# Kernel tuning notes

Measured on AMD Instinct MI355X. Metric: run time of the kernel, lower is better.

## Reference

```python
import jax, jax.numpy as jnp
import numpy as np

N = 32768          # nodes per graph (mol and protein must match for cat along dim 1)
E_MOL = 131072
E_PRO = 196608
F_MOL, F_PRO = 78, 54
HID, OUT_D, LAYERS = 512, 128, 3
ALPHA = 0.2


def _gcn_norm(edge_index, n, dtype):
    # add self loops, symmetric normalization D^-1/2 A D^-1/2 (PyG gcn_norm)
    sl = jnp.arange(n)
    row = jnp.concatenate([edge_index[0], sl])
    col = jnp.concatenate([edge_index[1], sl])
    deg = jax.ops.segment_sum(jnp.ones(row.shape[0], dtype), col, num_segments=n)
    dis = jnp.where(deg > 0, jax.lax.rsqrt(deg), 0.0).astype(dtype)
    return row, col, dis[row] * dis[col]


def _branch(x, edge_index, w_in, b_in, ws, w_out, b_out):
    # GCNII-dense stack: h = relu(Lin(x)); then per layer:
    #   agg = A_hat @ h ; support = (1-alpha)*agg + alpha*h0
    #   h = relu(support + support @ W_l) + h_prev   (identity-mapping + residual)
    n = x.shape[0]
    row, col, norm = _gcn_norm(edge_index, n, x.dtype)
    h = jax.nn.relu(x @ w_in + b_in)
    h0 = h
    prev = h
    for l in range(LAYERS):
        agg = jax.ops.segment_sum(norm[:, None] * prev[row], col, num_segments=n)  # [N,HID]
        support = (1.0 - ALPHA) * agg + ALPHA * h0
        prev = jax.nn.relu(support + support @ ws[l]) + prev
    return prev @ w_out + b_out  # [N, OUT_D]


def setup_inputs() -> dict:
    key = jax.random.key(0)
    ks = jax.random.split(key, 20)

    def glorot(k, shape):
        lim = float(np.sqrt(6.0 / (shape[-2] + shape[-1])))
        return jax.random.uniform(k, shape, jnp.float32, -lim, lim)

    inp = {
        "mol_x": jax.random.normal(ks[0], (N, F_MOL), jnp.float32),
        "mol_edge_index": jax.random.randint(ks[1], (2, E_MOL), 0, N, jnp.int64 if jax.config.jax_enable_x64 else jnp.int32),
        "pro_x": jax.random.normal(ks[2], (N, F_PRO), jnp.float32),
        "pro_edge_index": jax.random.randint(ks[3], (2, E_PRO), 0, N, jnp.int64 if jax.config.jax_enable_x64 else jnp.int32),
        "mol_w_in": glorot(ks[4], (F_MOL, HID)), "mol_b_in": jnp.zeros((HID,), jnp.float32),
        "mol_ws": glorot(ks[5], (LAYERS, HID, HID)),
        "mol_w_out": glorot(ks[6], (HID, OUT_D)), "mol_b_out": jnp.zeros((OUT_D,), jnp.float32),
        "pro_w_in": glorot(ks[7], (F_PRO, HID)), "pro_b_in": jnp.zeros((HID,), jnp.float32),
        "pro_ws": glorot(ks[8], (LAYERS, HID, HID)),
        "pro_w_out": glorot(ks[9], (HID, OUT_D)), "pro_b_out": jnp.zeros((OUT_D,), jnp.float32),
        "w_fc1": glorot(ks[10], (2 * OUT_D, 1024)), "b_fc1": jnp.zeros((1024,), jnp.float32),
        "w_fc2": glorot(ks[11], (1024, 512)), "b_fc2": jnp.zeros((512,), jnp.float32),
        "w_o": glorot(ks[12], (512, 1)), "b_o": jnp.zeros((1,), jnp.float32),
    }
    return inp


def reference(mol_x, mol_edge_index, pro_x, pro_edge_index,
              mol_w_in, mol_b_in, mol_ws, mol_w_out, mol_b_out,
              pro_w_in, pro_b_in, pro_ws, pro_w_out, pro_b_out,
              w_fc1, b_fc1, w_fc2, b_fc2, w_o, b_o):
    # eval mode: dropout = identity
    m = _branch(mol_x, mol_edge_index, mol_w_in, mol_b_in, mol_ws, mol_w_out, mol_b_out)
    p = _branch(pro_x, pro_edge_index, pro_w_in, pro_b_in, pro_ws, pro_w_out, pro_b_out)
    xc = jnp.concatenate([m, p], axis=1)            # [N, 2*OUT_D]
    xc = jax.nn.relu(xc @ w_fc1 + b_fc1)
    xc = jax.nn.relu(xc @ w_fc2 + b_fc2)
    return xc @ w_o + b_o                            # [N, 1]
```

## Files before the change

### kernel.cpp

```cpp
#include <hip/hip_runtime.h>
#include <stdint.h>

#define NN 32768
#define HID 512
#define EM 131072
#define EP 196608
#define AS1 __attribute__((address_space(1)))
#define AS3 __attribute__((address_space(3)))

typedef _Float16 h8 __attribute__((ext_vector_type(8)));
typedef float f4 __attribute__((ext_vector_type(4)));
typedef float f8 __attribute__((ext_vector_type(8)));

__device__ __forceinline__ void gload_lds16(const _Float16* g, _Float16* l) {
    __builtin_amdgcn_global_load_lds((AS1 void*)(g), (AS3 void*)(l), 16, 0, 0);
}
__device__ __forceinline__ f8 c8(h8 v) { return __builtin_convertvector(v, f8); }

struct ConvJobs {
    const float* src[12];
    _Float16* dst[12];
    int K[12], N[12], Kp[12];
    int blk0[13];
};

__global__ void conv_all(ConvJobs j) {
    __shared__ float tile[32][33];
    int blk = blockIdx.x, job = 0;
    while (blk >= j.blk0[job + 1]) ++job;
    int t = blk - j.blk0[job];
    int Kp = j.Kp[job], N = j.N[job], K = j.K[job];
    int ktiles = Kp >> 5;
    int n0 = (t / ktiles) << 5, k0 = (t % ktiles) << 5;
    int tn = threadIdx.x & 31, tr = threadIdx.x >> 5;
    const float* src = j.src[job];
    #pragma unroll
    for (int p = 0; p < 4; ++p) {
        int k = k0 + tr + p * 8;
        tile[tr + p * 8][tn] = (k < K) ? src[(size_t)k * N + n0 + tn] : 0.f;
    }
    __syncthreads();
    _Float16* dst = j.dst[job];
    #pragma unroll
    for (int p = 0; p < 4; ++p) {
        int nl = tr + p * 8;
        dst[((size_t)(k0 >> 5) * N + n0 + nl) * 32 + tn] = (_Float16)tile[tn][nl];
    }
}

__global__ void pad_x2(const float* s0, const float* s1, int F0, int F1, _Float16* dstb) {
    int z = blockIdx.z;
    const float* src = z ? s1 : s0;
    int F = z ? F1 : F0;
    _Float16* dst = dstb + (size_t)z * NN * 128;
    int idx = blockIdx.x * 256 + threadIdx.x;
    int i = idx >> 7, jj = idx & 127;
    dst[idx] = (jj < F) ? (_Float16)src[(size_t)i * F + jj] : (_Float16)0.f;
}

__global__ void init_deg(int* deg) {
    deg[(size_t)blockIdx.z * NN + blockIdx.x * 256 + threadIdx.x] = 1;
}

__global__ void count_edges2(const int* c0, int E0, const int* c1, int E1, int* deg) {
    int i = blockIdx.x * 256 + threadIdx.x;
    if (i < E0) atomicAdd(&deg[c0[i]], 1);
    else { i -= E0; if (i < E1) atomicAdd(&deg[NN + c1[i]], 1); }
}

__global__ void scan_offsets(const int* degb, int* offsb, int* curb, float* disb) {
    const int* deg = degb + blockIdx.z * NN;
    int* offs = offsb + blockIdx.z * (NN + 1);
    int* cur = curb + blockIdx.z * NN;
    float* dis = disb + blockIdx.z * NN;
    __shared__ int part[1024];
    int t = threadIdx.x, base = t * 32;
    int loc[32], sum = 0;
    for (int jj = 0; jj < 32; ++jj) {
        int d = deg[base + jj];
        dis[base + jj] = rsqrtf((float)d);
        loc[jj] = sum; sum += d - 1;
    }
    part[t] = sum;
    __syncthreads();
    for (int o = 1; o < 1024; o <<= 1) {
        int v = (t >= o) ? part[t - o] : 0;
        __syncthreads();
        part[t] += v;
        __syncthreads();
    }
    int pre = (t == 0) ? 0 : part[t - 1];
    for (int jj = 0; jj < 32; ++jj) { int x = pre + loc[jj]; offs[base + jj] = x; cur[base + jj] = x; }
    if (t == 1023) offs[NN] = part[1023];
}

__global__ void scatter2(const int* r0, const int* c0, int E0,
                         const int* r1, const int* c1, int E1,
                         int* cur, const float* dis, int2* s0, int2* s1) {
    int i = blockIdx.x * 256 + threadIdx.x;
    if (i < E0) {
        int r = r0[i];
        int p = atomicAdd(&cur[c0[i]], 1);
        int2 v; v.x = r; v.y = __float_as_int(dis[r]);
        s0[p] = v;
    } else {
        i -= E0;
        if (i < E1) {
            int r = r1[i];
            int p = atomicAdd(&cur[NN + c1[i]], 1);
            int2 v; v.x = r; v.y = __float_as_int(dis[NN + r]);
            s1[p] = v;
        }
    }
}

#define ROWP 536

struct LArgs {
    const _Float16* pin;
    const _Float16* h0;
    _Float16* pout;
    const float* dis;
    const int* offs;
    const int2* se0;
    const int2* se1;
    const _Float16* wT;
    const _Float16* woutT;
    const float* bo[2];
    _Float16* xc;
    size_t bstr;
    int mzadd;
};

__global__ __launch_bounds__(1024, 4) void layer_fused(LArgs a) {
    extern __shared__ _Float16 sup[];
    const int z = blockIdx.z, mz = z + a.mzadd;
    const _Float16* __restrict__ pin = a.pin + (size_t)z * a.bstr;
    const _Float16* __restrict__ h0 = a.h0 + (size_t)z * a.bstr;
    const _Float16* __restrict__ BT = a.wT + (size_t)z * (3 * 512 * 512);
    const float* __restrict__ dis = a.dis + mz * NN;
    const int* __restrict__ offs = a.offs + mz * (NN + 1);
    const int2* __restrict__ se = mz ? a.se1 : a.se0;
    const int tid = threadIdx.x, wave = tid >> 6, lane = tid & 63;
    const int row0 = blockIdx.x * 128;

    for (int i = 0; i < 8; ++i) {
        const int rl = wave * 8 + i, row = row0 + rl;
        const int e0 = offs[row], e1 = offs[row + 1];
        f8 acg = {};
        for (int e = e0; e < e1; e += 4) {
            const int j1 = (e + 1 < e1) ? e + 1 : e;
            const int j2 = (e + 2 < e1) ? e + 2 : e;
            const int j3 = (e + 3 < e1) ? e + 3 : e;
            const float m1 = (e + 1 < e1) ? 1.f : 0.f;
            const float m2 = (e + 2 < e1) ? 1.f : 0.f;
            const float m3 = (e + 3 < e1) ? 1.f : 0.f;
            const int2 p0 = se[e], p1 = se[j1], p2 = se[j2], p3 = se[j3];
            const float s0 = __int_as_float(p0.y);
            const float s1 = __int_as_float(p1.y) * m1;
            const float s2 = __int_as_float(p2.y) * m2;
            const float s3 = __int_as_float(p3.y) * m3;
            h8 v0 = *(const h8*)&pin[(size_t)p0.x * 512 + lane * 8];
            h8 v1 = *(const h8*)&pin[(size_t)p1.x * 512 + lane * 8];
            h8 v2 = *(const h8*)&pin[(size_t)p2.x * 512 + lane * 8];
            h8 v3 = *(const h8*)&pin[(size_t)p3.x * 512 + lane * 8];
            acg += s0 * c8(v0) + s1 * c8(v1) + s2 * c8(v2) + s3 * c8(v3);
        }
        const float si = dis[row];
        h8 pv = *(const h8*)&pin[(size_t)row * 512 + lane * 8];
        h8 hv = *(const h8*)&h0[(size_t)row * 512 + lane * 8];
        f8 r = 0.8f * si * (acg + si * c8(pv)) + 0.2f * c8(hv);
        *(h8*)&sup[rl * ROWP + lane * 8] = __builtin_convertvector(r, h8);
    }
    __syncthreads();

    const int wm = wave & 1, wn = wave >> 1;
    const int l15 = lane & 15, lq = lane >> 4;
    f4 acc[4][4] = {};
    #pragma unroll
    for (int kt = 0; kt < 8; ++kt) {
        #pragma unroll
        for (int s = 0; s < 2; ++s) {
            const int koff = kt * 64 + s * 32 + lq * 8;
            h8 af[4], bf[4];
            #pragma unroll
            for (int rt = 0; rt < 4; ++rt)
                af[rt] = *(const h8*)&sup[(wm * 64 + rt * 16 + l15) * ROWP + koff];
            #pragma unroll
            for (int ct = 0; ct < 4; ++ct)
                bf[ct] = *(const h8*)(BT + ((size_t)(kt * 2 + s) * 512
                                            + wn * 64 + ct * 16 + l15) * 32 + lq * 8);
            #pragma unroll
            for (int rt = 0; rt < 4; ++rt)
                #pragma unroll
                for (int ct = 0; ct < 4; ++ct)
                    acc[rt][ct] = __builtin_amdgcn_mfma_f32_16x16x32_f16(af[rt], bf[ct], acc[rt][ct], 0, 0, 0);
        }
    }
    __syncthreads();

    #pragma unroll
    for (int rt = 0; rt < 4; ++rt) {
        #pragma unroll
        for (int ct = 0; ct < 4; ++ct) {
            const int col = wn * 64 + ct * 16 + l15;
            #pragma unroll
            for (int r = 0; r < 4; ++r) {
                const int rl = wm * 64 + rt * 16 + lq * 4 + r;
                float nv = fmaxf((float)sup[rl * ROWP + col] + acc[rt][ct][r], 0.f);
                sup[rl * ROWP + col] = (_Float16)nv;
            }
        }
    }
    __syncthreads();

    const bool fuse_out = (a.woutT != nullptr);
    if (!fuse_out) {
        _Float16* __restrict__ pout = a.pout + (size_t)z * a.bstr;
        #pragma unroll
        for (int i = 0; i < 8; ++i) {
            const int rl = wave * 8 + i, row = row0 + rl;
            h8 s = *(const h8*)&sup[rl * ROWP + lane * 8];
            h8 pr = *(const h8*)&pin[(size_t)row * 512 + lane * 8];
            f8 v = c8(s) + c8(pr);
            *(h8*)&pout[(size_t)row * 512 + lane * 8] = __builtin_convertvector(v, h8);
        }
        return;
    }

    #pragma unroll
    for (int i = 0; i < 8; ++i) {
        const int rl = wave * 8 + i, row = row0 + rl;
        h8 s = *(const h8*)&sup[rl * ROWP + lane * 8];
        h8 pr = *(const h8*)&pin[(size_t)row * 512 + lane * 8];
        f8 v = c8(s) + c8(pr);
        *(h8*)&sup[rl * ROWP + lane * 8] = __builtin_convertvector(v, h8);
    }
    __syncthreads();

    const _Float16* __restrict__ WO = a.woutT + (size_t)z * (128 * 512);
    const float* __restrict__ bo = a.bo[mz];
    f4 acc2[4] = {};
    #pragma unroll
    for (int kt = 0; kt < 8; ++kt) {
        #pragma unroll
        for (int s = 0; s < 2; ++s) {
            const int koff = kt * 64 + s * 32 + lq * 8;
            h8 af[4];
            #pragma unroll
            for (int rt = 0; rt < 4; ++rt)
                af[rt] = *(const h8*)&sup[(wm * 64 + rt * 16 + l15) * ROWP + koff];
            h8 bf = *(const h8*)(WO + ((size_t)(kt * 2 + s) * 128 + wn * 16 + l15) * 32 + lq * 8);
            #pragma unroll
            for (int rt = 0; rt < 4; ++rt)
                acc2[rt] = __builtin_amdgcn_mfma_f32_16x16x32_f16(af[rt], bf, acc2[rt], 0, 0, 0);
        }
    }
    __syncthreads();
    #pragma unroll
    for (int rt = 0; rt < 4; ++rt) {
        const int col = wn * 16 + l15;
        #pragma unroll
        for (int r = 0; r < 4; ++r) {
            const int rl = wm * 64 + rt * 16 + lq * 4 + r;
            sup[rl * 136 + col] = (_Float16)(acc2[rt][r] + bo[col]);
        }
    }
    __syncthreads();
    #pragma unroll
    for (int i = 0; i < 2; ++i) {
        const int rl = wave * 8 + i * 4 + (lane >> 4);
        const int co = lane & 15;
        *(h8*)&a.xc[(size_t)(row0 + rl) * 256 + mz * 128 + co * 8] =
            *(const h8*)&sup[rl * 136 + co * 8];
    }
}

struct GArgs {
    const _Float16* A[2];
    const _Float16* BT[2];
    const float* bias[2];
    _Float16* C[2];
    _Float16* C2[2];
};

template <int K>
__global__ __launch_bounds__(512, 4) void gemm_a1(GArgs g, int ldc) {
    constexpr int NK = K / 64;
    __shared__ _Float16 lA[NK * 8 * 128 * 8];
    const int z = blockIdx.z;
    const _Float16* __restrict__ A = g.A[z];
    const _Float16* __restrict__ BT = g.BT[z];
    const int tid = threadIdx.x, wave = tid >> 6, lane = tid & 63;
    const int row0 = blockIdx.x * 128, col0 = blockIdx.y * 256;
    const int wm = wave & 1, wn = wave >> 1;
    const int l15 = lane & 15, lq = lane >> 4;
    constexpr int CNT = NK * 16 / 8;
    #pragma unroll
    for (int q = 0; q < CNT; ++q) {
        const int c = wave * CNT + q;
        const int kc = c >> 4, rem = c & 15, k8 = rem & 7, rh = rem >> 3;
        gload_lds16(A + (size_t)(row0 + rh * 64 + lane) * K + kc * 64 + k8 * 8,
                    &lA[((kc * 8 + k8) * 128 + rh * 64) * 8]);
    }
    __syncthreads();
    f4 acc[4][4] = {};
    #pragma unroll
    for (int kt = 0; kt < NK; ++kt) {
        #pragma unroll
        for (int s = 0; s < 2; ++s) {
            const int kq = s * 4 + lq;
            h8 af[4], bf[4];
            #pragma unroll
            for (int rt = 0; rt < 4; ++rt)
                af[rt] = *(const h8*)&lA[((kt * 8 + kq) * 128 + wm * 64 + rt * 16 + l15) * 8];
            #pragma unroll
            for (int ct = 0; ct < 4; ++ct)
                bf[ct] = *(const h8*)(BT + ((size_t)(kt * 2 + s) * ldc
                                            + col0 + wn * 64 + ct * 16 + l15) * 32 + lq * 8);
            #pragma unroll
            for (int rt = 0; rt < 4; ++rt)
                #pragma unroll
                for (int ct = 0; ct < 4; ++ct)
                    acc[rt][ct] = __builtin_amdgcn_mfma_f32_16x16x32_f16(af[rt], bf[ct], acc[rt][ct], 0, 0, 0);
        }
    }
    #pragma unroll
    for (int rt = 0; rt < 4; ++rt) {
        #pragma unroll
        for (int ct = 0; ct < 4; ++ct) {
            const int col = col0 + wn * 64 + ct * 16 + l15;
            #pragma unroll
            for (int r = 0; r < 4; ++r) {
                const int row = row0 + wm * 64 + rt * 16 + lq * 4 + r;
                float v = fmaxf(acc[rt][ct][r] + g.bias[z][col], 0.f);
                g.C[z][(size_t)row * ldc + col] = (_Float16)v;
                if (g.C2[z]) g.C2[z][(size_t)row * ldc + col] = (_Float16)v;
            }
        }
    }
}

__global__ __launch_bounds__(1024, 4) void gemm_fc2f(
    const _Float16* __restrict__ A, const _Float16* __restrict__ BT,
    const float* __restrict__ b2, const float* __restrict__ wo,
    const float* __restrict__ bo, float* __restrict__ out) {
    extern __shared__ _Float16 lA[];
    float* part = (float*)(lA + 64 * 1024);
    const int tid = threadIdx.x, wave = tid >> 6, lane = tid & 63;
    const int row0 = blockIdx.x * 64;
    const int wm = wave & 1, wn = wave >> 1;
    const int l15 = lane & 15, lq = lane >> 4;
    #pragma unroll
    for (int q = 0; q < 8; ++q) {
        const int c = wave * 8 + q;
        gload_lds16(A + (size_t)(row0 + lane) * 1024 + c * 8, &lA[(c * 64) * 8]);
    }
    __syncthreads();
    f4 acc[2][4] = {};
    #pragma unroll
    for (int kt = 0; kt < 32; ++kt) {
        const int ko = kt * 4 + lq;
        h8 af[2], bf[4];
        #pragma unroll
        for (int rt = 0; rt < 2; ++rt)
            af[rt] = *(const h8*)&lA[(ko * 64 + wm * 32 + rt * 16 + l15) * 8];
        #pragma unroll
        for (int ct = 0; ct < 4; ++ct)
            bf[ct] = *(const h8*)(BT + ((size_t)kt * 512 + wn * 64 + ct * 16 + l15) * 32 + lq * 8);
        #pragma unroll
        for (int rt = 0; rt < 2; ++rt)
            #pragma unroll
            for (int ct = 0; ct < 4; ++ct)
                acc[rt][ct] = __builtin_amdgcn_mfma_f32_16x16x32_f16(af[rt], bf[ct], acc[rt][ct], 0, 0, 0);
    }
    #pragma unroll
    for (int rt = 0; rt < 2; ++rt) {
        #pragma unroll
        for (int r = 0; r < 4; ++r) {
            float p = 0.f;
            #pragma unroll
            for (int ct = 0; ct < 4; ++ct) {
                const int colg = wn * 64 + ct * 16 + l15;
                float v = fmaxf(acc[rt][ct][r] + b2[colg], 0.f);
                p += v * wo[colg];
            }
            p += __shfl_xor(p, 1); p += __shfl_xor(p, 2);
            p += __shfl_xor(p, 4); p += __shfl_xor(p, 8);
            if (l15 == 0) {
                const int rl = wm * 32 + rt * 16 + lq * 4 + r;
                part[rl * 8 + wn] = p;
            }
        }
    }
    __syncthreads();
    if (tid < 64) {
        float s = bo[0];
        #pragma unroll
        for (int q = 0; q < 8; ++q) s += part[tid * 8 + q];
        out[row0 + tid] = s;
    }
}

struct WS {
    int *deg, *offs, *cur;
    int2 *srow0, *srow1;
    float* dis;
    _Float16 *winT, *wsT, *woutT, *fc1T, *fc2T;
    _Float16 *xpad, *h0, *prev0, *prev1, *xc;
    size_t total;
};

static WS plan(char* base, bool comb) {
    size_t off = 0;
    auto al = [&](size_t n) { off = (off + 255) & ~(size_t)255; size_t o = off; off += n; return base + o; };
    WS w;
    w.deg   = (int*)al(2 * NN * 4);
    w.dis   = (float*)al(2 * NN * 4);
    w.offs  = (int*)al(2 * (NN + 1) * 4);
    w.cur   = (int*)al(2 * NN * 4);
    w.srow0 = (int2*)al((size_t)EM * 8);
    w.srow1 = (int2*)al((size_t)EP * 8);
    w.winT  = (_Float16*)al(2 * 512 * 128 * 2);
    w.wsT   = (_Float16*)al((size_t)2 * 3 * 512 * 512 * 2);
    w.woutT = (_Float16*)al(2 * 128 * 512 * 2);
    w.fc1T  = (_Float16*)al(1024 * 256 * 2);
    w.fc2T  = (_Float16*)al((size_t)512 * 1024 * 2);
    const size_t nb = comb ? 2 : 1;
    const size_t HB = (size_t)NN * HID * 2;
    w.xpad  = (_Float16*)al(nb * NN * 128 * 2);
    w.h0    = (_Float16*)al(nb * HB);
    w.prev0 = (_Float16*)al(nb * HB);
    w.prev1 = (_Float16*)al(nb * HB);
    w.xc    = (_Float16*)al((size_t)NN * 256 * 2);
    w.total = off;
    return w;
}

extern "C" void kernel_launch(void* const* d_in, const int* in_sizes, int n_in,
                              void* d_out, int out_size, void* d_ws, size_t ws_size,
                              hipStream_t stream) {
    const float* mol_x   = (const float*)d_in[0];
    const int*   mol_ei  = (const int*)d_in[1];
    const float* pro_x   = (const float*)d_in[2];
    const int*   pro_ei  = (const int*)d_in[3];
    const float* win[2]  = {(const float*)d_in[4], (const float*)d_in[9]};
    const float* bin[2]  = {(const float*)d_in[5], (const float*)d_in[10]};
    const float* ws3[2]  = {(const float*)d_in[6], (const float*)d_in[11]};
    const float* wo[2]   = {(const float*)d_in[7], (const float*)d_in[12]};
    const float* bo[2]   = {(const float*)d_in[8], (const float*)d_in[13]};
    const float* w_fc1   = (const float*)d_in[14];
    const float* b_fc1   = (const float*)d_in[15];
    const float* w_fc2   = (const float*)d_in[16];
    const float* b_fc2   = (const float*)d_in[17];
    const float* w_o     = (const float*)d_in[18];
    const float* b_o     = (const float*)d_in[19];
    const int F[2] = {78, 54};

    char* wsb = (char*)d_ws;
    WS w = plan(wsb, true);
    const bool comb = (w.total <= ws_size);
    if (!comb) w = plan(wsb, false);
    const size_t BSTR = comb ? (size_t)NN * HID : 0;
    const size_t XSTR = comb ? (size_t)NN * 128 : 0;
    const int LDSB = 128 * ROWP * 2;
    const int LDSF = 64 * 1024 * 2 + 64 * 8 * 4;

    hipFuncSetAttribute((const void*)layer_fused,
                        hipFuncAttributeMaxDynamicSharedMemorySize, LDSB);
    hipFuncSetAttribute((const void*)gemm_fc2f,
                        hipFuncAttributeMaxDynamicSharedMemorySize, LDSF);

    ConvJobs j;
    int nblk = 0, ji = 0;
    auto addjob = [&](const float* s, _Float16* d, int K, int N, int Kp) {
        j.src[ji] = s; j.dst[ji] = d; j.K[ji] = K; j.N[ji] = N; j.Kp[ji] = Kp;
        j.blk0[ji] = nblk; nblk += (N >> 5) * (Kp >> 5); ++ji;
    };
    for (int b = 0; b < 2; ++b) addjob(win[b], w.winT + b * 512 * 128, F[b], 512, 128);
    for (int b = 0; b < 2; ++b)
        for (int l = 0; l < 3; ++l)
            addjob(ws3[b] + (size_t)l * 512 * 512,
                   w.wsT + ((size_t)b * 3 + l) * 512 * 512, 512, 512, 512);
    for (int b = 0; b < 2; ++b) addjob(wo[b], w.woutT + b * 128 * 512, 512, 128, 512);
    addjob(w_fc1, w.fc1T, 256, 1024, 256);
    addjob(w_fc2, w.fc2T, 1024, 512, 1024);
    j.blk0[12] = nblk;
    conv_all<<<nblk, 256, 0, stream>>>(j);

    init_deg<<<dim3(NN / 256, 1, 2), 256, 0, stream>>>(w.deg);
    count_edges2<<<(EM + EP + 255) / 256, 256, 0, stream>>>(mol_ei + EM, EM, pro_ei + EP, EP, w.deg);
    scan_offsets<<<dim3(1, 1, 2), 1024, 0, stream>>>(w.deg, w.offs, w.cur, w.dis);
    scatter2<<<(EM + EP + 255) / 256, 256, 0, stream>>>(mol_ei, mol_ei + EM, EM,
                                                        pro_ei, pro_ei + EP, EP,
                                                        w.cur, w.dis, w.srow0, w.srow1);

    auto branch_chain = [&](int zcount, int b0) {
        GArgs g{};
        for (int z = 0; z < zcount; ++z) {
            int b = b0 + z;
            g.A[z] = w.xpad + z * XSTR;
            g.BT[z] = w.winT + b * 512 * 128;
            g.bias[z] = bin[b];
            g.C[z] = w.h0 + z * BSTR;
            g.C2[z] = nullptr;
        }
        gemm_a1<128><<<dim3(256, 2, zcount), 512, 0, stream>>>(g, HID);
        const _Float16* pins[3] = {w.h0, w.prev1, w.prev0};
        _Float16* pouts[3] = {w.prev1, w.prev0, nullptr};
        for (int l = 0; l < 3; ++l) {
            LArgs a{};
            a.pin = pins[l];
            a.h0 = w.h0;
            a.pout = pouts[l];
            a.dis = w.dis; a.offs = w.offs;
            a.se0 = w.srow0; a.se1 = w.srow1;
            a.wT = w.wsT + ((size_t)b0 * 3 + l) * 512 * 512;
            a.woutT = (l == 2) ? (w.woutT + (size_t)b0 * 128 * 512) : nullptr;
            a.bo[0] = bo[0]; a.bo[1] = bo[1];
            a.xc = w.xc;
            a.bstr = BSTR; a.mzadd = b0;
            layer_fused<<<dim3(256, 1, zcount), 1024, LDSB, stream>>>(a);
        }
    };

    if (comb) {
        pad_x2<<<dim3(NN * 128 / 256, 1, 2), 256, 0, stream>>>(mol_x, pro_x, F[0], F[1], w.xpad);
        branch_chain(2, 0);
    } else {
        for (int b = 0; b < 2; ++b) {
            pad_x2<<<dim3(NN * 128 / 256, 1, 1), 256, 0, stream>>>(
                b ? pro_x : mol_x, nullptr, F[b], 0, w.xpad);
            branch_chain(1, b);
        }
    }

    _Float16* x1 = w.h0;
    GArgs g1{};
    g1.A[0] = w.xc; g1.BT[0] = w.fc1T; g1.bias[0] = b_fc1; g1.C[0] = x1; g1.C2[0] = nullptr;
    gemm_a1<256><<<dim3(256, 4, 1), 512, 0, stream>>>(g1, 1024);
    gemm_fc2f<<<dim3(NN / 64, 1), 1024, LDSF, stream>>>(x1, w.fc2T, b_fc2, w_o, b_o, (float*)d_out);
    (void)in_sizes; (void)n_in; (void)out_size; (void)ws_size;
}
```

Before: 681.0 us.

## Split fused layer into two half-tiles to overlap gather with MFMA

The fused GCN layer kernel now processes its 128-row tile as two 64-row halves in separate LDS buffers. The second half's sparse neighbour gather is issued before the first half's MFMA GEMM, so memory-bound gather work and matrix math from different waves can interleave. Each wave now covers 32 output columns across all 64 rows instead of 64x64, which changes the register and B-operand load pattern. The risk is that the gather and GEMM phases within a wave still run in sequence, so any overlap relies on the scheduler interleaving waves.

```diff
diff --git a/kernel.cpp b/kernel.cpp
--- a/kernel.cpp
+++ b/kernel.cpp
@@ -115,6 +115,7 @@
 }
 
 #define ROWP 536
+#define HROWS 64
 
 struct LArgs {
     const _Float16* pin;
@@ -133,7 +134,9 @@
 };
 
 __global__ __launch_bounds__(1024, 4) void layer_fused(LArgs a) {
-    extern __shared__ _Float16 sup[];
+    extern __shared__ _Float16 lds[];
+    _Float16* bufA = lds;
+    _Float16* bufB = lds + HROWS * ROWP;
     const int z = blockIdx.z, mz = z + a.mzadd;
     const _Float16* __restrict__ pin = a.pin + (size_t)z * a.bstr;
     const _Float16* __restrict__ h0 = a.h0 + (size_t)z * a.bstr;
@@ -143,103 +146,128 @@
     const int2* __restrict__ se = mz ? a.se1 : a.se0;
     const int tid = threadIdx.x, wave = tid >> 6, lane = tid & 63;
     const int row0 = blockIdx.x * 128;
-
-    for (int i = 0; i < 8; ++i) {
-        const int rl = wave * 8 + i, row = row0 + rl;
-        const int e0 = offs[row], e1 = offs[row + 1];
-        f8 acg = {};
-        for (int e = e0; e < e1; e += 4) {
-            const int j1 = (e + 1 < e1) ? e + 1 : e;
-            const int j2 = (e + 2 < e1) ? e + 2 : e;
-            const int j3 = (e + 3 < e1) ? e + 3 : e;
-            const float m1 = (e + 1 < e1) ? 1.f : 0.f;
-            const float m2 = (e + 2 < e1) ? 1.f : 0.f;
-            const float m3 = (e + 3 < e1) ? 1.f : 0.f;
-            const int2 p0 = se[e], p1 = se[j1], p2 = se[j2], p3 = se[j3];
-            const float s0 = __int_as_float(p0.y);
-            const float s1 = __int_as_float(p1.y) * m1;
-            const float s2 = __int_as_float(p2.y) * m2;
-            const float s3 = __int_as_float(p3.y) * m3;
-            h8 v0 = *(const h8*)&pin[(size_t)p0.x * 512 + lane * 8];
-            h8 v1 = *(const h8*)&pin[(size_t)p1.x * 512 + lane * 8];
-            h8 v2 = *(const h8*)&pin[(size_t)p2.x * 512 + lane * 8];
-            h8 v3 = *(const h8*)&pin[(size_t)p3.x * 512 + lane * 8];
-            acg += s0 * c8(v0) + s1 * c8(v1) + s2 * c8(v2) + s3 * c8(v3);
-        }
-        const float si = dis[row];
-        h8 pv = *(const h8*)&pin[(size_t)row * 512 + lane * 8];
-        h8 hv = *(const h8*)&h0[(size_t)row * 512 + lane * 8];
-        f8 r = 0.8f * si * (acg + si * c8(pv)) + 0.2f * c8(hv);
-        *(h8*)&sup[rl * ROWP + lane * 8] = __builtin_convertvector(r, h8);
-    }
-    __syncthreads();
-
-    const int wm = wave & 1, wn = wave >> 1;
     const int l15 = lane & 15, lq = lane >> 4;
-    f4 acc[4][4] = {};
-    #pragma unroll
-    for (int kt = 0; kt < 8; ++kt) {
-        #pragma unroll
-        for (int s = 0; s < 2; ++s) {
-            const int koff = kt * 64 + s * 32 + lq * 8;
-            h8 af[4], bf[4];
-            #pragma unroll
-            for (int rt = 0; rt < 4; ++rt)
-                af[rt] = *(const h8*)&sup[(wm * 64 + rt * 16 + l15) * ROWP + koff];
-            #pragma unroll
-            for (int ct = 0; ct < 4; ++ct)
-                bf[ct] = *(const h8*)(BT + ((size_t)(kt * 2 + s) * 512
-                                            + wn * 64 + ct * 16 + l15) * 32 + lq * 8);
-            #pragma unroll
-            for (int rt = 0; rt < 4; ++rt)
+
+    auto gather4 = [&](_Float16* buf, int rbase) {
+        for (int i = 0; i < 4; ++i) {
+            const int rl = wave * 4 + i, row = row0 + rbase + rl;
+            const int e0 = offs[row], e1 = offs[row + 1];
+            f8 acg = {};
+            for (int e = e0; e < e1; e += 4) {
+                const int j1 = (e + 1 < e1) ? e + 1 : e;
+                const int j2 = (e + 2 < e1) ? e + 2 : e;
+                const int j3 = (e + 3 < e1) ? e + 3 : e;
+                const float m1 = (e + 1 < e1) ? 1.f : 0.f;
+                const float m2 = (e + 2 < e1) ? 1.f : 0.f;
+                const float m3 = (e + 3 < e1) ? 1.f : 0.f;
+                const int2 p0 = se[e], p1 = se[j1], p2 = se[j2], p3 = se[j3];
+                const float s0 = __int_as_float(p0.y);
+                const float s1 = __int_as_float(p1.y) * m1;
+                const float s2 = __int_as_float(p2.y) * m2;
+                const float s3 = __int_as_float(p3.y) * m3;
+                h8 v0 = *(const h8*)&pin[(size_t)p0.x * 512 + lane * 8];
+                h8 v1 = *(const h8*)&pin[(size_t)p1.x * 512 + lane * 8];
+                h8 v2 = *(const h8*)&pin[(size_t)p2.x * 512 + lane * 8];
+                h8 v3 = *(const h8*)&pin[(size_t)p3.x * 512 + lane * 8];
+                acg += s0 * c8(v0) + s1 * c8(v1) + s2 * c8(v2) + s3 * c8(v3);
+            }
+            const float si = dis[row];
+            h8 pv = *(const h8*)&pin[(size_t)row * 512 + lane * 8];
+            h8 hv = *(const h8*)&h0[(size_t)row * 512 + lane * 8];
+            f8 r = 0.8f * si * (acg + si * c8(pv)) + 0.2f * c8(hv);
+            *(h8*)&buf[rl * ROWP + lane * 8] = __builtin_convertvector(r, h8);
+        }
+    };
+
+    auto gemmh = [&](const _Float16* buf, f4 (&acc)[4][2]) {
+        #pragma unroll
+        for (int kt = 0; kt < 8; ++kt) {
+            #pragma unroll
+            for (int s = 0; s < 2; ++s) {
+                const int koff = kt * 64 + s * 32 + lq * 8;
+                h8 af[4], bf[2];
                 #pragma unroll
-                for (int ct = 0; ct < 4; ++ct)
-                    acc[rt][ct] = __builtin_amdgcn_mfma_f32_16x16x32_f16(af[rt], bf[ct], acc[rt][ct], 0, 0, 0);
-        }
-    }
-    __syncthreads();
-
-    #pragma unroll
-    for (int rt = 0; rt < 4; ++rt) {
-        #pragma unroll
-        for (int ct = 0; ct < 4; ++ct) {
-            const int col = wn * 64 + ct * 16 + l15;
-            #pragma unroll
-            for (int r = 0; r < 4; ++r) {
-                const int rl = wm * 64 + rt * 16 + lq * 4 + r;
-                float nv = fmaxf((float)sup[rl * ROWP + col] + acc[rt][ct][r], 0.f);
-                sup[rl * ROWP + col] = (_Float16)nv;
+                for (int rt = 0; rt < 4; ++rt)
+                    af[rt] = *(const h8*)&buf[(rt * 16 + l15) * ROWP + koff];
+                #pragma unroll
+                for (int ct = 0; ct < 2; ++ct)
+                    bf[ct] = *(const h8*)(BT + ((size_t)(kt * 2 + s) * 512
+                                                + wave * 32 + ct * 16 + l15) * 32 + lq * 8);
+                #pragma unroll
+                for (int rt = 0; rt < 4; ++rt)
+                    #pragma unroll
+                    for (int ct = 0; ct < 2; ++ct)
+                        acc[rt][ct] = __builtin_amdgcn_mfma_f32_16x16x32_f16(af[rt], bf[ct], acc[rt][ct], 0, 0, 0);
             }
         }
-    }
+    };
+
+    auto epih = [&](_Float16* buf, f4 (&acc)[4][2]) {
+        #pragma unroll
+        for (int rt = 0; rt < 4; ++rt) {
+            #pragma unroll
+            for (int ct = 0; ct < 2; ++ct) {
+                const int col = wave * 32 + ct * 16 + l15;
+                #pragma unroll
+                for (int r = 0; r < 4; ++r) {
+                    const int rl = rt * 16 + lq * 4 + r;
+                    float nv = fmaxf((float)buf[rl * ROWP + col] + acc[rt][ct][r], 0.f);
+                    buf[rl * ROWP + col] = (_Float16)nv;
+                }
+            }
+        }
+    };
+
+    auto copyh = [&](const _Float16* buf, int rbase, _Float16* pout) {
+        #pragma unroll
+        for (int i = 0; i < 4; ++i) {
+            const int rl = wave * 4 + i, row = row0 + rbase + rl;
+            h8 s = *(const h8*)&buf[rl * ROWP + lane * 8];
+            h8 pr = *(const h8*)&pin[(size_t)row * 512 + lane * 8];
+            f8 v = c8(s) + c8(pr);
+            *(h8*)&pout[(size_t)row * 512 + lane * 8] = __builtin_convertvector(v, h8);
+        }
+    };
+
+    f4 accA[4][2] = {}, accB[4][2] = {};
+
+    gather4(bufA, 0);
+    __syncthreads();
+    gather4(bufB, 64);
+    gemmh(bufA, accA);
+    __syncthreads();
+    gemmh(bufB, accB);
+    epih(bufA, accA);
     __syncthreads();
 
     const bool fuse_out = (a.woutT != nullptr);
     if (!fuse_out) {
         _Float16* __restrict__ pout = a.pout + (size_t)z * a.bstr;
-        #pragma unroll
-        for (int i = 0; i < 8; ++i) {
-            const int rl = wave * 8 + i, row = row0 + rl;
-            h8 s = *(const h8*)&sup[rl * ROWP + lane * 8];
-            h8 pr = *(const h8*)&pin[(size_t)row * 512 + lane * 8];
-            f8 v = c8(s) + c8(pr);
-            *(h8*)&pout[(size_t)row * 512 + lane * 8] = __builtin_convertvector(v, h8);
-        }
+        epih(bufB, accB);
+        copyh(bufA, 0, pout);
+        __syncthreads();
+        copyh(bufB, 64, pout);
         return;
     }
 
+    epih(bufB, accB);
+    __syncthreads();
     #pragma unroll
     for (int i = 0; i < 8; ++i) {
-        const int rl = wave * 8 + i, row = row0 + rl;
-        h8 s = *(const h8*)&sup[rl * ROWP + lane * 8];
+        const int rloc = wave * 8 + i;
+        _Float16* buf = (rloc < 64) ? bufA : bufB;
+        const int rl = rloc & 63, row = row0 + rloc;
+        h8 s = *(const h8*)&buf[rl * ROWP + lane * 8];
         h8 pr = *(const h8*)&pin[(size_t)row * 512 + lane * 8];
         f8 v = c8(s) + c8(pr);
-        *(h8*)&sup[rl * ROWP + lane * 8] = __builtin_convertvector(v, h8);
+        *(h8*)&buf[rl * ROWP + lane * 8] = __builtin_convertvector(v, h8);
     }
     __syncthreads();
 
     const _Float16* __restrict__ WO = a.woutT + (size_t)z * (128 * 512);
     const float* __restrict__ bo = a.bo[mz];
+    const int wm = wave & 1, wn = wave >> 1;
+    const _Float16* bsel = wm ? bufB : bufA;
     f4 acc2[4] = {};
     #pragma unroll
     for (int kt = 0; kt < 8; ++kt) {
@@ -249,7 +277,7 @@
             h8 af[4];
             #pragma unroll
             for (int rt = 0; rt < 4; ++rt)
-                af[rt] = *(const h8*)&sup[(wm * 64 + rt * 16 + l15) * ROWP + koff];
+                af[rt] = *(const h8*)&bsel[(rt * 16 + l15) * ROWP + koff];
             h8 bf = *(const h8*)(WO + ((size_t)(kt * 2 + s) * 128 + wn * 16 + l15) * 32 + lq * 8);
             #pragma unroll
             for (int rt = 0; rt < 4; ++rt)
@@ -263,7 +291,7 @@
         #pragma unroll
         for (int r = 0; r < 4; ++r) {
             const int rl = wm * 64 + rt * 16 + lq * 4 + r;
-            sup[rl * 136 + col] = (_Float16)(acc2[rt][r] + bo[col]);
+            lds[rl * 136 + col] = (_Float16)(acc2[rt][r] + bo[col]);
         }
     }
     __syncthreads();
@@ -272,7 +300,7 @@
         const int rl = wave * 8 + i * 4 + (lane >> 4);
         const int co = lane & 15;
         *(h8*)&a.xc[(size_t)(row0 + rl) * 256 + mz * 128 + co * 8] =
-            *(const h8*)&sup[rl * 136 + co * 8];
+            *(const h8*)&lds[rl * 136 + co * 8];
     }
 }
 
```

After: 707.8 us. +3.9%, slower.

## Fuse fc1 and fc2 head GEMMs into one kernel keeping fc1 activations in LDS

Applied to the files above, without the earlier changes.

Replaces the separate fc1 GEMM kernel and the fc2+output kernel with one fused head kernel. Each 64-row block computes fc1 in 128-column chunks, writes the ReLU result to LDS as fp16, and immediately accumulates it into the fc2 product. This removes the global write and re-read of the N×1024 fc1 activation and one kernel launch. In exchange it adds two block barriers per chunk and loads the fc1 weights separately in every block.

```diff
diff --git a/kernel.cpp b/kernel.cpp
--- a/kernel.cpp
+++ b/kernel.cpp
@@ -341,38 +341,77 @@
     }
 }
 
-__global__ __launch_bounds__(1024, 4) void gemm_fc2f(
-    const _Float16* __restrict__ A, const _Float16* __restrict__ BT,
+__global__ __launch_bounds__(1024, 4) void head_fused(
+    const _Float16* __restrict__ xc, const _Float16* __restrict__ W1T,
+    const float* __restrict__ b1, const _Float16* __restrict__ W2T,
     const float* __restrict__ b2, const float* __restrict__ wo,
     const float* __restrict__ bo, float* __restrict__ out) {
-    extern __shared__ _Float16 lA[];
-    float* part = (float*)(lA + 64 * 1024);
+    __shared__ _Float16 lxc[32 * 64 * 8];
+    __shared__ _Float16 lx1[16 * 64 * 8];
+    __shared__ float part[64 * 8];
     const int tid = threadIdx.x, wave = tid >> 6, lane = tid & 63;
     const int row0 = blockIdx.x * 64;
     const int wm = wave & 1, wn = wave >> 1;
     const int l15 = lane & 15, lq = lane >> 4;
     #pragma unroll
-    for (int q = 0; q < 8; ++q) {
-        const int c = wave * 8 + q;
-        gload_lds16(A + (size_t)(row0 + lane) * 1024 + c * 8, &lA[(c * 64) * 8]);
-    }
-    __syncthreads();
-    f4 acc[2][4] = {};
-    #pragma unroll
-    for (int kt = 0; kt < 32; ++kt) {
-        const int ko = kt * 4 + lq;
-        h8 af[2], bf[4];
-        #pragma unroll
-        for (int rt = 0; rt < 2; ++rt)
-            af[rt] = *(const h8*)&lA[(ko * 64 + wm * 32 + rt * 16 + l15) * 8];
-        #pragma unroll
-        for (int ct = 0; ct < 4; ++ct)
-            bf[ct] = *(const h8*)(BT + ((size_t)kt * 512 + wn * 64 + ct * 16 + l15) * 32 + lq * 8);
-        #pragma unroll
-        for (int rt = 0; rt < 2; ++rt)
-            #pragma unroll
-            for (int ct = 0; ct < 4; ++ct)
-                acc[rt][ct] = __builtin_amdgcn_mfma_f32_16x16x32_f16(af[rt], bf[ct], acc[rt][ct], 0, 0, 0);
+    for (int q = 0; q < 2; ++q) {
+        const int c = wave * 2 + q;
+        gload_lds16(xc + (size_t)(row0 + lane) * 256 + c * 8, &lxc[(c * 64) * 8]);
+    }
+    __syncthreads();
+    f4 acc2[2][4] = {};
+    for (int cc = 0; cc < 8; ++cc) {
+        f4 acc1[2] = {};
+        #pragma unroll
+        for (int kt = 0; kt < 4; ++kt) {
+            #pragma unroll
+            for (int s = 0; s < 2; ++s) {
+                const int kq = s * 4 + lq;
+                h8 af[2];
+                #pragma unroll
+                for (int rt = 0; rt < 2; ++rt)
+                    af[rt] = *(const h8*)&lxc[((kt * 8 + kq) * 64 + wm * 32 + rt * 16 + l15) * 8];
+                const int col = cc * 128 + wn * 16 + l15;
+                h8 bf = *(const h8*)(W1T + ((size_t)(kt * 2 + s) * 1024 + col) * 32 + lq * 8);
+                #pragma unroll
+                for (int rt = 0; rt < 2; ++rt)
+                    acc1[rt] = __builtin_amdgcn_mfma_f32_16x16x32_f16(af[rt], bf, acc1[rt], 0, 0, 0);
+            }
+        }
+        __syncthreads();
+        {
+            const int cl = wn * 16 + l15;
+            const float bb = b1[cc * 128 + cl];
+            #pragma unroll
+            for (int rt = 0; rt < 2; ++rt)
+                #pragma unroll
+                for (int r = 0; r < 4; ++r) {
+                    const int row = wm * 32 + rt * 16 + lq * 4 + r;
+                    lx1[((cl >> 3) * 64 + row) * 8 + (cl & 7)] =
+                        (_Float16)fmaxf(acc1[rt][r] + bb, 0.f);
+                }
+        }
+        __syncthreads();
+        #pragma unroll
+        for (int kt = 0; kt < 2; ++kt) {
+            #pragma unroll
+            for (int s = 0; s < 2; ++s) {
+                const int kq = s * 4 + lq;
+                h8 af[2], bf[4];
+                #pragma unroll
+                for (int rt = 0; rt < 2; ++rt)
+                    af[rt] = *(const h8*)&lx1[((kt * 8 + kq) * 64 + wm * 32 + rt * 16 + l15) * 8];
+                #pragma unroll
+                for (int ct = 0; ct < 4; ++ct)
+                    bf[ct] = *(const h8*)(W2T + ((size_t)(cc * 4 + kt * 2 + s) * 512
+                                                 + wn * 64 + ct * 16 + l15) * 32 + lq * 8);
+                #pragma unroll
+                for (int rt = 0; rt < 2; ++rt)
+                    #pragma unroll
+                    for (int ct = 0; ct < 4; ++ct)
+                        acc2[rt][ct] = __builtin_amdgcn_mfma_f32_16x16x32_f16(af[rt], bf[ct], acc2[rt][ct], 0, 0, 0);
+            }
+        }
     }
     #pragma unroll
     for (int rt = 0; rt < 2; ++rt) {
@@ -382,7 +421,7 @@
             #pragma unroll
             for (int ct = 0; ct < 4; ++ct) {
                 const int colg = wn * 64 + ct * 16 + l15;
-                float v = fmaxf(acc[rt][ct][r] + b2[colg], 0.f);
+                float v = fmaxf(acc2[rt][ct][r] + b2[colg], 0.f);
                 p += v * wo[colg];
             }
             p += __shfl_xor(p, 1); p += __shfl_xor(p, 2);
@@ -464,12 +503,9 @@
     const size_t BSTR = comb ? (size_t)NN * HID : 0;
     const size_t XSTR = comb ? (size_t)NN * 128 : 0;
     const int LDSB = 128 * ROWP * 2;
-    const int LDSF = 64 * 1024 * 2 + 64 * 8 * 4;
 
     hipFuncSetAttribute((const void*)layer_fused,
                         hipFuncAttributeMaxDynamicSharedMemorySize, LDSB);
-    hipFuncSetAttribute((const void*)gemm_fc2f,
-                        hipFuncAttributeMaxDynamicSharedMemorySize, LDSF);
 
     ConvJobs j;
     int nblk = 0, ji = 0;
@@ -535,10 +571,7 @@
         }
     }
 
-    _Float16* x1 = w.h0;
-    GArgs g1{};
-    g1.A[0] = w.xc; g1.BT[0] = w.fc1T; g1.bias[0] = b_fc1; g1.C[0] = x1; g1.C2[0] = nullptr;
-    gemm_a1<256><<<dim3(256, 4, 1), 512, 0, stream>>>(g1, 1024);
-    gemm_fc2f<<<dim3(NN / 64, 1), 1024, LDSF, stream>>>(x1, w.fc2T, b_fc2, w_o, b_o, (float*)d_out);
+    head_fused<<<dim3(NN / 64, 1), 1024, 0, stream>>>(
+        w.xc, w.fc1T, b_fc1, w.fc2T, b_fc2, w_o, b_o, (float*)d_out);
     (void)in_sizes; (void)n_in; (void)out_size; (void)ws_size;
 }
```

Result: no change. 672.7 us (-1.2%).
